# Kernel tuning notes

Hardware: AMD Instinct MI355X
Metric: run time of the kernel (lower is better)

## Reference

```python
import jax, jax.numpy as jnp
import numpy as np

N, E = 50000, 300000
IN_DIM, CODE_DIM = 1024, 768
HID, HEADS, DH = 256, 4, 64
NUM_REL = 5
CODE_WEIGHT = 1.0


def setup_inputs() -> dict:
    key = jax.random.key(0)
    ks = jax.random.split(key, 24)
    p = lambda k, shape: jax.random.normal(k, shape, dtype=jnp.float32) * 0.05
    return {
        "x": jax.random.normal(ks[0], (N, IN_DIM), dtype=jnp.float32),
        "edge_index": jax.random.randint(ks[1], (2, E), 0, N, dtype=jnp.int64),
        "edge_type": jax.random.randint(ks[2], (E,), 0, NUM_REL, dtype=jnp.int64),
        "edge_weight": jax.random.uniform(ks[3], (E,), dtype=jnp.float32),
        "rel_emb": p(ks[4], (NUM_REL, HID)),
        "W_in": p(ks[5], (HID, IN_DIM)),
        "b_in": jnp.zeros((HID,), jnp.float32),
        "W1": p(ks[6], (HEADS * DH, HID)),
        "a1_src": p(ks[7], (HEADS, DH)),
        "a1_dst": p(ks[8], (HEADS, DH)),
        "b1": jnp.zeros((HEADS * DH,), jnp.float32),
        "W2": p(ks[9], (HEADS * DH, HID)),
        "a2_src": p(ks[10], (HEADS, DH)),
        "a2_dst": p(ks[11], (HEADS, DH)),
        "b2": jnp.zeros((HEADS * DH,), jnp.float32),
        "ln1_g": jnp.ones((HID,), jnp.float32),
        "ln1_b": jnp.zeros((HID,), jnp.float32),
        "ln2_g": jnp.ones((HID,), jnp.float32),
        "ln2_b": jnp.zeros((HID,), jnp.float32),
        "W_out": p(ks[12], (1, HID)),
        "b_out": jnp.zeros((1,), jnp.float32),
    }


def _layer_norm(x, g, b, eps=1e-5):
    m = x.mean(-1, keepdims=True)
    v = ((x - m) ** 2).mean(-1, keepdims=True)
    return (x - m) * jax.lax.rsqrt(v + eps) * g + b


def _gat_conv(h, s_all, d_all, W, a_src, a_dst, bias):
    # PyG GATConv (concat=True, negative_slope=0.2), self-loops already in s_all/d_all
    xh = (h @ W.T).reshape(N, HEADS, DH)                      # [N,H,DH]
    al_s = (xh * a_src).sum(-1)                                # [N,H]
    al_d = (xh * a_dst).sum(-1)                                # [N,H]
    e = jax.nn.leaky_relu(al_s[s_all] + al_d[d_all], 0.2)      # [E+N,H]
    mx = jax.ops.segment_max(e, d_all, num_segments=N)         # segment softmax over dst
    ex = jnp.exp(e - mx[d_all])
    den = jax.ops.segment_sum(ex, d_all, num_segments=N)
    alpha = ex / (den[d_all] + 1e-16)
    out = jax.ops.segment_sum(xh[s_all] * alpha[:, :, None], d_all, num_segments=N)
    return out.reshape(N, HEADS * DH) + bias


def reference(x, edge_index, edge_type, edge_weight, rel_emb, W_in, b_in,
              W1, a1_src, a1_dst, b1, W2, a2_src, a2_dst, b2,
              ln1_g, ln1_b, ln2_g, ln2_b, W_out, b_out):
    # split (code_at_front=True), standardize numeric, l2-normalize code
    x_code = x[:, :CODE_DIM]
    x_num = x[:, CODE_DIM:]
    m = x_num.mean(0, keepdims=True)
    s = jnp.maximum(x_num.std(0, ddof=1, keepdims=True), 1e-6)
    x_num = (x_num - m) / s
    nrm = jnp.maximum(jnp.linalg.norm(x_code, axis=1, keepdims=True), 1e-12)
    x_code = x_code / nrm
    xin = jnp.concatenate([x_num, CODE_WEIGHT * x_code], axis=-1)

    h = jax.nn.relu(xin @ W_in.T + b_in)                       # [N,HID]

    src, dst = edge_index[0], edge_index[1]
    rel = rel_emb[edge_type] * edge_weight[:, None]            # [E,HID]
    msg = h[src] + rel
    h = h.at[dst].add(msg)                                     # index_add

    loop = jnp.arange(N, dtype=src.dtype)                      # GATConv add_self_loops
    s_all = jnp.concatenate([src, loop])
    d_all = jnp.concatenate([dst, loop])

    h1 = _gat_conv(h, s_all, d_all, W1, a1_src, a1_dst, b1)
    h = _layer_norm(h1 + h, ln1_g, ln1_b)
    h2 = _gat_conv(h, s_all, d_all, W2, a2_src, a2_dst, b2)
    h = _layer_norm(h2 + h, ln2_g, ln2_b)
    return (h @ W_out.T + b_out).squeeze(-1)                   # [N]
```

## Files before the change

kernel.cpp:

```cpp
#include <hip/hip_runtime.h>
#include <math.h>

constexpr int NN   = 50000;
constexpr int EE   = 300000;
constexpr int IND  = 1024;
constexpr int CODE = 768;
constexpr int HID  = 256;

typedef __bf16 bf16_t;
typedef bf16_t bf16x4 __attribute__((ext_vector_type(4)));
typedef bf16_t bf16x8 __attribute__((ext_vector_type(8)));
typedef float  f32x4  __attribute__((ext_vector_type(4)));

__device__ __forceinline__ f32x4 mfma16(bf16x8 a, bf16x8 b, f32x4 c) {
    return __builtin_amdgcn_mfma_f32_16x16x32_bf16(a, b, c, 0, 0, 0);
}

#define GLOAD_LDS16(gp, lp) __builtin_amdgcn_global_load_lds(                         \
    (__attribute__((address_space(1))) void*)(gp),                                    \
    (__attribute__((address_space(3))) void*)(lp), 16, 0, 0)

__device__ __forceinline__ void cvt_split(f32x4 u0, f32x4 u1, bf16x8& hi, bf16x8& lo) {
    #pragma unroll
    for (int i = 0; i < 4; i++) {
        bf16_t h0 = (bf16_t)u0[i];
        hi[i]     = h0;
        lo[i]     = (bf16_t)(u0[i] - (float)h0);
        bf16_t h1 = (bf16_t)u1[i];
        hi[4 + i] = h1;
        lo[4 + i] = (bf16_t)(u1[i] - (float)h1);
    }
}

__device__ __forceinline__ f32x4 ld_bf4(const bf16_t* p) {
    bf16x4 v = *(const bf16x4*)p;
    f32x4 r;
    r[0] = (float)v[0]; r[1] = (float)v[1]; r[2] = (float)v[2]; r[3] = (float)v[3];
    return r;
}

__global__ void colstats_kernel(const float* __restrict__ x, float* __restrict__ sums) {
    int col = threadIdx.x;
    float s = 0.f, s2 = 0.f;
    for (int row = blockIdx.x; row < NN; row += gridDim.x) {
        float v = x[(size_t)row * IND + CODE + col];
        s += v; s2 += v * v;
    }
    atomicAdd(&sums[col], s);
    atomicAdd(&sums[256 + col], s2);
}

__global__ void rownorm_kernel(const float* __restrict__ x, float* __restrict__ invnorm) {
    int lane = threadIdx.x & 63;
    int wid  = threadIdx.x >> 6;
    int row  = blockIdx.x * 4 + wid;
    if (row >= NN) return;
    const float4* x4 = (const float4*)(x + (size_t)row * IND);
    float s = 0.f;
    #pragma unroll
    for (int i = 0; i < 3; i++) {
        float4 v = x4[lane + i * 64];
        s += v.x * v.x + v.y * v.y + v.z * v.z + v.w * v.w;
    }
    #pragma unroll
    for (int off = 32; off; off >>= 1) s += __shfl_xor(s, off);
    if (lane == 0) invnorm[row] = 1.f / fmaxf(sqrtf(s), 1e-12f);
}

__global__ void prep_w_kernel(const float* __restrict__ W, const float* __restrict__ sums,
                              const float* __restrict__ b_in, bf16_t* __restrict__ Wh,
                              float* __restrict__ cb)
{
    int c = blockIdx.x, t = threadIdx.x;
    float mean = sums[t] / (float)NN;
    float var  = (sums[256 + t] - (float)NN * mean * mean) / (float)(NN - 1);
    float sd   = fmaxf(sqrtf(fmaxf(var, 0.f)), 1e-6f);
    float invstd = 1.f / sd;

    const float* wr = W + (size_t)c * IND;
    bf16_t* wh = Wh + (size_t)c * IND;
    for (int k = t; k < 768; k += 256) wh[k] = (bf16_t)wr[256 + k];
    wh[768 + t] = (bf16_t)(wr[t] * invstd);

    float p = wr[t] * invstd * mean;
    #pragma unroll
    for (int off = 32; off; off >>= 1) p += __shfl_xor(p, off);
    __shared__ float ps[4];
    if ((t & 63) == 0) ps[t >> 6] = p;
    __syncthreads();
    if (t == 0) cb[c] = b_in[c] - (ps[0] + ps[1] + ps[2] + ps[3]);
}

__global__ void prep_ws_kernel(const float* __restrict__ W1, const float* __restrict__ W2,
                               bf16_t* __restrict__ Wh1, bf16_t* __restrict__ Wh2)
{
    int c = blockIdx.x, t = threadIdx.x;
    if (c < 256) Wh1[(size_t)c * 256 + t] = (bf16_t)W1[(size_t)c * 256 + t];
    else {
        int cc = c - 256;
        Wh2[(size_t)cc * 256 + t] = (bf16_t)W2[(size_t)cc * 256 + t];
    }
}


__device__ __forceinline__ void stage_a(const float* __restrict__ src, int ldk,
                                        int rowbase, int maxrow, int k0,
                                        float* ldsbuf, int tid) {
    int w = tid >> 6, l = tid & 63;
    int lr = l >> 3, lc = l & 7;
    int g  = lc ^ lr;
    #pragma unroll
    for (int i = 0; i < 4; i++) {
        int rloc = i * 32 + w * 8;
        float* dst = ldsbuf + rloc * 32;
        int row = rowbase + rloc + lr;
        if (row > maxrow) row = maxrow;
        const float* gp = src + (size_t)row * ldk + k0 + g * 4;
        GLOAD_LDS16(gp, dst);
    }
}

__device__ __forceinline__ void stage_b(const bf16_t* __restrict__ src, int n0, int ldk,
                                        int maxrow, int k0, bf16_t* buf, int tid) {
    int w = tid >> 6, l = tid & 63;
    #pragma unroll
    for (int i = 0; i < 2; i++) {
        int gbase = w * 128 + i * 64;
        bf16_t* dst = buf + gbase * 8;
        int g = gbase + l;
        int col = g >> 2, p = g & 3;
        int gs = p ^ ((col >> 1) & 3);
        int row = n0 + col;
        if (row > maxrow) row = maxrow;
        const bf16_t* gp = src + (size_t)row * ldk + k0 + gs * 8;
        GLOAD_LDS16(gp, dst);
    }
}

template<int MODE, int K, int FATTN>
__global__ __launch_bounds__(256) void gemm_mfma_kernel(
    const float* __restrict__ A, const bf16_t* __restrict__ A16,
    const bf16_t* __restrict__ Bh, const float* __restrict__ cb,
    const float* __restrict__ invnorm, const float* __restrict__ a_src,
    const float* __restrict__ a_dst, float* __restrict__ out,
    bf16_t* __restrict__ xhb, float* __restrict__ al_s, float* __restrict__ al_d)
{
    constexpr int ASZF = (MODE == 1) ? 2 * 128 * 32 : 8;
    constexpr int ASZB = (MODE == 0) ? 2 * 128 * 32 : 8;
    __shared__ float  Asf[ASZF];
    __shared__ bf16_t Asb[ASZB];
    __shared__ bf16_t Bhs[2][128 * 32];
    __shared__ float inv_s[128];
    constexpr int NT = K / 32;

    int tid  = threadIdx.x;
    int lane = tid & 63;
    int w    = tid >> 6;
    int wr   = w >> 1, wc = w & 1;
    int r0   = blockIdx.x * 128, n0 = blockIdx.y * 128;

    if (MODE == 1 && tid < 128) {
        int r = r0 + tid;
        inv_s[tid] = (r < NN) ? invnorm[r] : 1.f;
    }

    f32x4 acc[4][4];
    #pragma unroll
    for (int i = 0; i < 4; i++)
        #pragma unroll
        for (int j = 0; j < 4; j++) acc[i][j] = (f32x4)0.f;

    int kc = lane >> 4, fr = lane & 15;

    if (MODE == 1) stage_a(A, K, r0, NN - 1, 0, Asf, tid);
    else           stage_b(A16, r0, K, NN - 1, 0, Asb, tid);
    stage_b(Bh, n0, K, 255, 0, Bhs[0], tid);
    __syncthreads();

    for (int t = 0; t < NT; ++t) {
        int buf = t & 1;
        if (t + 1 < NT) {
            if (MODE == 1) stage_a(A, K, r0, NN - 1, (t + 1) * 32, Asf + (buf ^ 1) * (128 * 32), tid);
            else           stage_b(A16, r0, K, NN - 1, (t + 1) * 32, Asb + (buf ^ 1) * (128 * 32), tid);
            stage_b(Bh, n0, K, 255, (t + 1) * 32, Bhs[buf ^ 1], tid);
        }
        if (MODE == 1 && t == 24) {
            #pragma unroll
            for (int mf = 0; mf < 4; mf++) {
                f32x4 iv = *(const f32x4*)&inv_s[wr * 64 + mf * 16 + kc * 4];
                #pragma unroll
                for (int nf = 0; nf < 4; nf++)
                    #pragma unroll
                    for (int j = 0; j < 4; j++) acc[mf][nf][j] *= iv[j];
            }
        }
        const bf16_t* Hb = Bhs[buf];
        bf16x8 ahi[4], alo[4];
        #pragma unroll
        for (int mf = 0; mf < 4; mf++) {
            int r = wr * 64 + mf * 16 + fr;
            if (MODE == 1) {
                const float* Ab = Asf + buf * (128 * 32);
                int rb = r * 32, r7 = r & 7;
                f32x4 u0 = *(const f32x4*)&Ab[rb + (((2 * kc + 0) ^ r7) << 2)];
                f32x4 u1 = *(const f32x4*)&Ab[rb + (((2 * kc + 1) ^ r7) << 2)];
                cvt_split(u0, u1, ahi[mf], alo[mf]);
            } else {
                const bf16_t* Ab = Asb + buf * (128 * 32);
                int pr = kc ^ ((r >> 1) & 3);
                ahi[mf] = *(const bf16x8*)&Ab[r * 32 + pr * 8];
            }
        }
        #pragma unroll
        for (int nf = 0; nf < 4; nf++) {
            int c  = wc * 64 + nf * 16 + fr;
            int pr = kc ^ ((c >> 1) & 3);
            bf16x8 bhi = *(const bf16x8*)&Hb[c * 32 + pr * 8];
            #pragma unroll
            for (int mf = 0; mf < 4; mf++) {
                acc[mf][nf] = mfma16(ahi[mf], bhi, acc[mf][nf]);
                if (MODE == 1) acc[mf][nf] = mfma16(alo[mf], bhi, acc[mf][nf]);
            }
        }
        __syncthreads();
    }

    int head = blockIdx.y * 2 + wc;
    float asv[4], adv[4];
    if (FATTN) {
        #pragma unroll
        for (int nf = 0; nf < 4; nf++) {
            asv[nf] = a_src[head * 64 + nf * 16 + fr];
            adv[nf] = a_dst[head * 64 + nf * 16 + fr];
        }
    }
    #pragma unroll
    for (int mf = 0; mf < 4; mf++) {
        #pragma unroll
        for (int j = 0; j < 4; j++) {
            int row = r0 + wr * 64 + mf * 16 + kc * 4 + j;
            bool ok = row < NN;
            float s = 0.f, d = 0.f;
            #pragma unroll
            for (int nf = 0; nf < 4; nf++) {
                int col = n0 + wc * 64 + nf * 16 + fr;
                float v = acc[mf][nf][j];
                if (MODE == 1) {
                    v = fmaxf(v + cb[col], 0.f);
                    if (ok) out[(size_t)row * HID + col] = v;
                }
                if (FATTN) {
                    s += v * asv[nf]; d += v * adv[nf];
                    if (ok) xhb[(size_t)row * HID + col] = (bf16_t)v;
                }
            }
            if (FATTN) {
                #pragma unroll
                for (int off = 1; off < 16; off <<= 1) {
                    s += __shfl_xor(s, off);
                    d += __shfl_xor(d, off);
                }
                if (ok && fr == 0) {
                    al_s[row * 4 + head] = s;
                    al_d[row * 4 + head] = d;
                }
            }
        }
    }
}

__global__ void deg_kernel(const int* __restrict__ ei, int* __restrict__ deg) {
    int e = blockIdx.x * 256 + threadIdx.x;
    if (e < EE) atomicAdd(&deg[ei[EE + e]], 1);
}

constexpr int SCB = 1024;
constexpr int SCN = (NN + SCB - 1) / SCB;

__global__ void scan_pass1(const int* __restrict__ deg, int* __restrict__ bsum) {
    int b = blockIdx.x, t = threadIdx.x;
    int base = b * SCB + t * 4;
    int s = 0;
    #pragma unroll
    for (int i = 0; i < 4; i++) { int idx = base + i; if (idx < NN) s += deg[idx]; }
    #pragma unroll
    for (int off = 32; off; off >>= 1) s += __shfl_xor(s, off);
    __shared__ int ps[4];
    if ((t & 63) == 0) ps[t >> 6] = s;
    __syncthreads();
    if (t == 0) bsum[b] = ps[0] + ps[1] + ps[2] + ps[3];
}

__global__ void scan_pass2(int* __restrict__ bsum) {
    int t = threadIdx.x;
    int orig = (t < SCN) ? bsum[t] : 0;
    int v = orig;
    for (int off = 1; off < 64; off <<= 1) {
        int u = __shfl_up(v, off);
        if (t >= off) v += u;
    }
    if (t < SCN) bsum[t] = v - orig;
}

__global__ void scan_pass3(const int* __restrict__ deg, const int* __restrict__ boffs,
                           int* __restrict__ row_ptr, int* __restrict__ cursor) {
    int b = blockIdx.x, t = threadIdx.x;
    int base = b * SCB + t * 4;
    int d[4]; int tot = 0;
    #pragma unroll
    for (int i = 0; i < 4; i++) { int idx = base + i; d[i] = (idx < NN) ? deg[idx] : 0; tot += d[i]; }
    int v = tot;
    for (int off = 1; off < 64; off <<= 1) {
        int u = __shfl_up(v, off);
        if ((t & 63) >= off) v += u;
    }
    __shared__ int wsum[4];
    if ((t & 63) == 63) wsum[t >> 6] = v;
    __syncthreads();
    int woff = 0;
    for (int j = 0; j < (t >> 6); j++) woff += wsum[j];
    int run = boffs[b] + woff + v - tot;
    #pragma unroll
    for (int i = 0; i < 4; i++) {
        int idx = base + i;
        if (idx < NN) {
            cursor[idx] = run;
            run += d[i];
            row_ptr[idx + 1] = run;
        }
    }
    if (b == 0 && t == 0) row_ptr[0] = 0;
}

__global__ void fill_kernel(const int* __restrict__ ei, const int* __restrict__ etype,
                            const float* __restrict__ ew, int* __restrict__ cursor,
                            int* __restrict__ csr_src, int* __restrict__ csr_t,
                            float* __restrict__ csr_w) {
    int e = blockIdx.x * 256 + threadIdx.x;
    if (e >= EE) return;
    int dst = ei[EE + e];
    int pos = atomicAdd(&cursor[dst], 1);
    csr_src[pos] = ei[e];
    csr_t[pos]   = etype[e];
    csr_w[pos]   = ew[e];
}

__global__ void relagg_kernel(const float* __restrict__ h, const int* __restrict__ row_ptr,
                              const int* __restrict__ csr_src, const int* __restrict__ csr_t,
                              const float* __restrict__ csr_w,
                              const float* __restrict__ rel_emb, float* __restrict__ out,
                              bf16_t* __restrict__ out16)
{
    int lane = threadIdx.x & 63, wid = threadIdx.x >> 6;
    int node = blockIdx.x * 4 + wid;
    if (node >= NN) return;
    int c0 = lane * 4;
    f32x4 acc = *(const f32x4*)(h + (size_t)node * HID + c0);
    float wsum[5] = {0.f, 0.f, 0.f, 0.f, 0.f};
    int beg = row_ptr[node], end = row_ptr[node + 1];
    for (int k = beg; k < end; k += 8) {
        int s[8], tt[8]; float ww[8], vm[8];
        #pragma unroll
        for (int j = 0; j < 8; j++) {
            int kk = k + j;
            bool valid = kk < end;
            kk = valid ? kk : (end - 1);
            s[j]  = csr_src[kk];
            tt[j] = csr_t[kk];
            ww[j] = valid ? csr_w[kk] : 0.f;
            vm[j] = valid ? 1.f : 0.f;
        }
        f32x4 xv[8];
        #pragma unroll
        for (int j = 0; j < 8; j++) xv[j] = *(const f32x4*)(h + (size_t)s[j] * HID + c0);
        #pragma unroll
        for (int j = 0; j < 8; j++) {
            acc += vm[j] * xv[j];
            #pragma unroll
            for (int r = 0; r < 5; r++) wsum[r] += (tt[j] == r) ? ww[j] : 0.f;
        }
    }
    #pragma unroll
    for (int r = 0; r < 5; r++)
        acc += wsum[r] * *(const f32x4*)(rel_emb + r * HID + c0);
    *(f32x4*)(out + (size_t)node * HID + c0) = acc;
    bf16x4 a16;
    #pragma unroll
    for (int i = 0; i < 4; i++) a16[i] = (bf16_t)acc[i];
    *(bf16x4*)(out16 + (size_t)node * HID + c0) = a16;
}

template<int FINAL>
__global__ void gat_kernel(const bf16_t* __restrict__ xhb, const float* __restrict__ al_s,
                           const float* __restrict__ al_d, const int* __restrict__ row_ptr,
                           const int* __restrict__ csr_src, const float* __restrict__ h_res,
                           const float* __restrict__ bias, const float* __restrict__ ln_g,
                           const float* __restrict__ ln_b, float* __restrict__ out,
                           bf16_t* __restrict__ out16,
                           const float* __restrict__ W_out, const float* __restrict__ b_out,
                           float* __restrict__ final_out)
{
    int lane = threadIdx.x & 63, wid = threadIdx.x >> 6;
    int node = blockIdx.x * 4 + wid;
    if (node >= NN) return;
    int hh = lane >> 4;
    int c0 = lane * 4;

    float ald = al_d[node * 4 + hh];
    float m, den;
    f32x4 acc;

    {
        float als = al_s[node * 4 + hh];
        float e = als + ald;
        e = (e >= 0.f) ? e : 0.2f * e;
        m = e; den = 1.f;
        acc = ld_bf4(xhb + (size_t)node * HID + c0);
    }

    int beg = row_ptr[node], end = row_ptr[node + 1];
    for (int k = beg; k < end; k += 8) {
        int s[8]; float als[8];
        #pragma unroll
        for (int j = 0; j < 8; j++) {
            int kk = k + j;
            bool valid = kk < end;
            s[j] = csr_src[valid ? kk : (end - 1)];
            als[j] = valid ? 0.f : -INFINITY;
        }
        #pragma unroll
        for (int j = 0; j < 8; j++)
            if (als[j] == 0.f) als[j] = al_s[s[j] * 4 + hh];
        f32x4 xv[8];
        #pragma unroll
        for (int j = 0; j < 8; j++) xv[j] = ld_bf4(xhb + (size_t)s[j] * HID + c0);
        #pragma unroll
        for (int j = 0; j < 8; j++) {
            float e = als[j] + ald;
            e = (e >= 0.f) ? e : 0.2f * e;
            float mn  = fmaxf(m, e);
            float f   = __expf(m - mn);
            float wgt = __expf(e - mn);
            m   = mn;
            den = den * f + wgt;
            acc = acc * f + wgt * xv[j];
        }
    }

    f32x4 bia = *(const f32x4*)(bias + c0);
    f32x4 res = *(const f32x4*)(h_res + (size_t)node * HID + c0);
    f32x4 z;
    float rd = 1.f / (den + 1e-16f);
    #pragma unroll
    for (int i = 0; i < 4; i++) z[i] = acc[i] * rd + bia[i] + res[i];

    float s = z[0] + z[1] + z[2] + z[3];
    #pragma unroll
    for (int off = 32; off; off >>= 1) s += __shfl_xor(s, off);
    float mean = s * (1.f / 256.f);
    float vp = 0.f;
    #pragma unroll
    for (int i = 0; i < 4; i++) { float d2 = z[i] - mean; vp += d2 * d2; }
    #pragma unroll
    for (int off = 32; off; off >>= 1) vp += __shfl_xor(vp, off);
    float rstd = rsqrtf(vp * (1.f / 256.f) + 1e-5f);

    f32x4 g = *(const f32x4*)(ln_g + c0);
    f32x4 bb = *(const f32x4*)(ln_b + c0);
    if (FINAL) {
        f32x4 wo = *(const f32x4*)(W_out + c0);
        float dot = 0.f;
        #pragma unroll
        for (int i = 0; i < 4; i++)
            dot += ((z[i] - mean) * rstd * g[i] + bb[i]) * wo[i];
        #pragma unroll
        for (int off = 32; off; off >>= 1) dot += __shfl_xor(dot, off);
        if (lane == 0) final_out[node] = dot + b_out[0];
    } else {
        f32x4 o;
        bf16x4 o16;
        #pragma unroll
        for (int i = 0; i < 4; i++) {
            o[i] = (z[i] - mean) * rstd * g[i] + bb[i];
            o16[i] = (bf16_t)o[i];
        }
        *(f32x4*)(out + (size_t)node * HID + c0) = o;
        *(bf16x4*)(out16 + (size_t)node * HID + c0) = o16;
    }
}

extern "C" void kernel_launch(void* const* d_in, const int* in_sizes, int n_in,
                              void* d_out, int out_size, void* d_ws, size_t ws_size,
                              hipStream_t stream) {
    const float* x       = (const float*)d_in[0];
    const int*   ei      = (const int*)d_in[1];
    const int*   etype   = (const int*)d_in[2];
    const float* ew      = (const float*)d_in[3];
    const float* rel_emb = (const float*)d_in[4];
    const float* W_in    = (const float*)d_in[5];
    const float* b_in    = (const float*)d_in[6];
    const float* W1      = (const float*)d_in[7];
    const float* a1s     = (const float*)d_in[8];
    const float* a1d     = (const float*)d_in[9];
    const float* b1      = (const float*)d_in[10];
    const float* W2      = (const float*)d_in[11];
    const float* a2s     = (const float*)d_in[12];
    const float* a2d     = (const float*)d_in[13];
    const float* b2      = (const float*)d_in[14];
    const float* ln1g    = (const float*)d_in[15];
    const float* ln1b    = (const float*)d_in[16];
    const float* ln2g    = (const float*)d_in[17];
    const float* ln2b    = (const float*)d_in[18];
    const float* W_out   = (const float*)d_in[19];
    const float* b_out   = (const float*)d_in[20];
    float* out = (float*)d_out;

    char* ws = (char*)d_ws;
    auto alloc = [&](size_t bytes) {
        void* p = (void*)ws;
        ws += (bytes + 255) & ~(size_t)255;
        return p;
    };
    float*  bufA     = (float*)alloc((size_t)NN * HID * 4);
    float*  bufB     = (float*)alloc((size_t)NN * HID * 4);
    bf16_t* xhb      = (bf16_t*)alloc((size_t)NN * HID * 2);
    bf16_t* gin16    = (bf16_t*)alloc((size_t)NN * HID * 2);
    bf16_t* wmh      = (bf16_t*)alloc((size_t)HID * IND * 2);
    bf16_t* w1h      = (bf16_t*)alloc((size_t)HID * HID * 2);
    bf16_t* w2h      = (bf16_t*)alloc((size_t)HID * HID * 2);
    float*  cbv      = (float*)alloc(256 * 4);
    float*  stats_s  = (float*)alloc(512 * 4);
    float*  invnorm  = (float*)alloc((size_t)NN * 4);
    float*  al_s     = (float*)alloc((size_t)NN * 4 * 4);
    float*  al_d     = (float*)alloc((size_t)NN * 4 * 4);
    int*    deg      = (int*)alloc((size_t)NN * 4);
    int*    row_ptr  = (int*)alloc((size_t)(NN + 1) * 4);
    int*    cursor   = (int*)alloc((size_t)NN * 4);
    int*    csr_src  = (int*)alloc((size_t)EE * 4);
    int*    csr_t    = (int*)alloc((size_t)EE * 4);
    float*  csr_w    = (float*)alloc((size_t)EE * 4);
    int*    bsum     = (int*)alloc(64 * 4);

    hipMemsetAsync(stats_s, 0, 512 * 4, stream);
    hipMemsetAsync(deg, 0, (size_t)NN * 4, stream);

    colstats_kernel<<<1024, 256, 0, stream>>>(x, stats_s);
    rownorm_kernel<<<(NN + 3) / 4, 256, 0, stream>>>(x, invnorm);
    prep_w_kernel<<<256, 256, 0, stream>>>(W_in, stats_s, b_in, wmh, cbv);
    prep_ws_kernel<<<512, 256, 0, stream>>>(W1, W2, w1h, w2h);

    deg_kernel<<<(EE + 255) / 256, 256, 0, stream>>>(ei, deg);
    scan_pass1<<<SCN, 256, 0, stream>>>(deg, bsum);
    scan_pass2<<<1, 64, 0, stream>>>(bsum);
    scan_pass3<<<SCN, 256, 0, stream>>>(deg, bsum, row_ptr, cursor);
    fill_kernel<<<(EE + 255) / 256, 256, 0, stream>>>(ei, etype, ew, cursor,
                                                      csr_src, csr_t, csr_w);

    dim3 g1((NN + 127) / 128, 2);

    gemm_mfma_kernel<1, 1024, 0><<<g1, 256, 0, stream>>>(
        x, nullptr, wmh, cbv, invnorm, nullptr, nullptr, bufA, nullptr, nullptr, nullptr);

    int nodeBlocks = (NN + 3) / 4;

    relagg_kernel<<<nodeBlocks, 256, 0, stream>>>(bufA, row_ptr, csr_src, csr_t, csr_w,
                                                  rel_emb, bufB, gin16);

    gemm_mfma_kernel<0, 256, 1><<<g1, 256, 0, stream>>>(
        nullptr, gin16, w1h, nullptr, nullptr, a1s, a1d, nullptr, xhb, al_s, al_d);
    gat_kernel<0><<<nodeBlocks, 256, 0, stream>>>(xhb, al_s, al_d, row_ptr, csr_src,
                                                  bufB, b1, ln1g, ln1b, bufA, gin16,
                                                  nullptr, nullptr, nullptr);

    gemm_mfma_kernel<0, 256, 1><<<g1, 256, 0, stream>>>(
        nullptr, gin16, w2h, nullptr, nullptr, a2s, a2d, nullptr, xhb, al_s, al_d);
    gat_kernel<1><<<nodeBlocks, 256, 0, stream>>>(xhb, al_s, al_d, row_ptr, csr_src,
                                                  bufA, b2, ln2g, ln2b, nullptr, nullptr,
                                                  W_out, b_out, out);
}
```

Before: 427.7 us.

## Pre-normalize input to bf16 and drop split-precision MFMA in input GEMM

A new xin_kernel applies the row L2 norm to the code columns and column standardization to the numeric columns, writing a bf16 copy of the input with the numeric block placed first. The input projection GEMM then streams bf16 A tiles with single MFMAs, where it previously loaded fp32 tiles and did hi/lo split conversion with two MFMAs per fragment. Folding the stats into the weights and bias is dropped, and the weight conversions are merged into one kernel. This trades an extra read of x plus a bf16 write and re-read of about 100 MB against halving MFMA work and fp32 A traffic, and it lowers input precision to plain bf16.

```diff
diff --git a/kernel.cpp b/kernel.cpp
--- a/kernel.cpp
+++ b/kernel.cpp
@@ -19,18 +19,6 @@
 #define GLOAD_LDS16(gp, lp) __builtin_amdgcn_global_load_lds(                         \
     (__attribute__((address_space(1))) void*)(gp),                                    \
     (__attribute__((address_space(3))) void*)(lp), 16, 0, 0)
-
-__device__ __forceinline__ void cvt_split(f32x4 u0, f32x4 u1, bf16x8& hi, bf16x8& lo) {
-    #pragma unroll
-    for (int i = 0; i < 4; i++) {
-        bf16_t h0 = (bf16_t)u0[i];
-        hi[i]     = h0;
-        lo[i]     = (bf16_t)(u0[i] - (float)h0);
-        bf16_t h1 = (bf16_t)u1[i];
-        hi[4 + i] = h1;
-        lo[4 + i] = (bf16_t)(u1[i] - (float)h1);
-    }
-}
 
 __device__ __forceinline__ f32x4 ld_bf4(const bf16_t* p) {
     bf16x4 v = *(const bf16x4*)p;
@@ -50,75 +38,63 @@
     atomicAdd(&sums[256 + col], s2);
 }
 
-__global__ void rownorm_kernel(const float* __restrict__ x, float* __restrict__ invnorm) {
-    int lane = threadIdx.x & 63;
-    int wid  = threadIdx.x >> 6;
+__global__ void xin_kernel(const float* __restrict__ x, const float* __restrict__ sums,
+                           bf16_t* __restrict__ xin)
+{
+    int lane = threadIdx.x & 63, wid = threadIdx.x >> 6;
     int row  = blockIdx.x * 4 + wid;
     if (row >= NN) return;
-    const float4* x4 = (const float4*)(x + (size_t)row * IND);
+    const f32x4* x4 = (const f32x4*)(x + (size_t)row * IND);
+    f32x4 v[4];
+    #pragma unroll
+    for (int i = 0; i < 4; i++) v[i] = x4[lane + 64 * i];
     float s = 0.f;
     #pragma unroll
+    for (int i = 0; i < 3; i++)
+        s += v[i][0] * v[i][0] + v[i][1] * v[i][1] + v[i][2] * v[i][2] + v[i][3] * v[i][3];
+    #pragma unroll
+    for (int off = 32; off; off >>= 1) s += __shfl_xor(s, off);
+    float inr = 1.f / fmaxf(sqrtf(s), 1e-12f);
+
+    bf16_t* xr = xin + (size_t)row * IND;
+    #pragma unroll
     for (int i = 0; i < 3; i++) {
-        float4 v = x4[lane + i * 64];
-        s += v.x * v.x + v.y * v.y + v.z * v.z + v.w * v.w;
-    }
-    #pragma unroll
-    for (int off = 32; off; off >>= 1) s += __shfl_xor(s, off);
-    if (lane == 0) invnorm[row] = 1.f / fmaxf(sqrtf(s), 1e-12f);
-}
-
-__global__ void prep_w_kernel(const float* __restrict__ W, const float* __restrict__ sums,
-                              const float* __restrict__ b_in, bf16_t* __restrict__ Wh,
-                              float* __restrict__ cb)
+        bf16x4 o;
+        #pragma unroll
+        for (int q = 0; q < 4; q++) o[q] = (bf16_t)(v[i][q] * inr);
+        *(bf16x4*)(xr + 256 + 4 * (lane + 64 * i)) = o;
+    }
+    {
+        bf16x4 o;
+        #pragma unroll
+        for (int q = 0; q < 4; q++) {
+            int j = 4 * lane + q;
+            float mean = sums[j] / (float)NN;
+            float var  = (sums[256 + j] - (float)NN * mean * mean) / (float)(NN - 1);
+            float invstd = 1.f / fmaxf(sqrtf(fmaxf(var, 0.f)), 1e-6f);
+            o[q] = (bf16_t)((v[3][q] - mean) * invstd);
+        }
+        *(bf16x4*)(xr + 4 * lane) = o;
+    }
+}
+
+__global__ void prep_all_kernel(const float* __restrict__ W_in, const float* __restrict__ W1,
+                                const float* __restrict__ W2, bf16_t* __restrict__ Wmh,
+                                bf16_t* __restrict__ Wh1, bf16_t* __restrict__ Wh2)
 {
-    int c = blockIdx.x, t = threadIdx.x;
-    float mean = sums[t] / (float)NN;
-    float var  = (sums[256 + t] - (float)NN * mean * mean) / (float)(NN - 1);
-    float sd   = fmaxf(sqrtf(fmaxf(var, 0.f)), 1e-6f);
-    float invstd = 1.f / sd;
-
-    const float* wr = W + (size_t)c * IND;
-    bf16_t* wh = Wh + (size_t)c * IND;
-    for (int k = t; k < 768; k += 256) wh[k] = (bf16_t)wr[256 + k];
-    wh[768 + t] = (bf16_t)(wr[t] * invstd);
-
-    float p = wr[t] * invstd * mean;
-    #pragma unroll
-    for (int off = 32; off; off >>= 1) p += __shfl_xor(p, off);
-    __shared__ float ps[4];
-    if ((t & 63) == 0) ps[t >> 6] = p;
-    __syncthreads();
-    if (t == 0) cb[c] = b_in[c] - (ps[0] + ps[1] + ps[2] + ps[3]);
-}
-
-__global__ void prep_ws_kernel(const float* __restrict__ W1, const float* __restrict__ W2,
-                               bf16_t* __restrict__ Wh1, bf16_t* __restrict__ Wh2)
-{
-    int c = blockIdx.x, t = threadIdx.x;
-    if (c < 256) Wh1[(size_t)c * 256 + t] = (bf16_t)W1[(size_t)c * 256 + t];
-    else {
-        int cc = c - 256;
-        Wh2[(size_t)cc * 256 + t] = (bf16_t)W2[(size_t)cc * 256 + t];
-    }
-}
-
-
-__device__ __forceinline__ void stage_a(const float* __restrict__ src, int ldk,
-                                        int rowbase, int maxrow, int k0,
-                                        float* ldsbuf, int tid) {
-    int w = tid >> 6, l = tid & 63;
-    int lr = l >> 3, lc = l & 7;
-    int g  = lc ^ lr;
-    #pragma unroll
-    for (int i = 0; i < 4; i++) {
-        int rloc = i * 32 + w * 8;
-        float* dst = ldsbuf + rloc * 32;
-        int row = rowbase + rloc + lr;
-        if (row > maxrow) row = maxrow;
-        const float* gp = src + (size_t)row * ldk + k0 + g * 4;
-        GLOAD_LDS16(gp, dst);
-    }
-}
+    int b = blockIdx.x, t = threadIdx.x;
+    if (b < 1024) {
+        size_t i = (size_t)b * 256 + t;
+        Wmh[i] = (bf16_t)W_in[i];
+    } else if (b < 1280) {
+        size_t i = (size_t)(b - 1024) * 256 + t;
+        Wh1[i] = (bf16_t)W1[i];
+    } else {
+        size_t i = (size_t)(b - 1280) * 256 + t;
+        Wh2[i] = (bf16_t)W2[i];
+    }
+}
+
 
 __device__ __forceinline__ void stage_b(const bf16_t* __restrict__ src, int n0, int ldk,
                                         int maxrow, int k0, bf16_t* buf, int tid) {
@@ -139,18 +115,13 @@
 
 template<int MODE, int K, int FATTN>
 __global__ __launch_bounds__(256) void gemm_mfma_kernel(
-    const float* __restrict__ A, const bf16_t* __restrict__ A16,
-    const bf16_t* __restrict__ Bh, const float* __restrict__ cb,
-    const float* __restrict__ invnorm, const float* __restrict__ a_src,
+    const bf16_t* __restrict__ A16, const bf16_t* __restrict__ Bh,
+    const float* __restrict__ bin, const float* __restrict__ a_src,
     const float* __restrict__ a_dst, float* __restrict__ out,
     bf16_t* __restrict__ xhb, float* __restrict__ al_s, float* __restrict__ al_d)
 {
-    constexpr int ASZF = (MODE == 1) ? 2 * 128 * 32 : 8;
-    constexpr int ASZB = (MODE == 0) ? 2 * 128 * 32 : 8;
-    __shared__ float  Asf[ASZF];
-    __shared__ bf16_t Asb[ASZB];
+    __shared__ bf16_t Asb[2][128 * 32];
     __shared__ bf16_t Bhs[2][128 * 32];
-    __shared__ float inv_s[128];
     constexpr int NT = K / 32;
 
     int tid  = threadIdx.x;
@@ -159,11 +130,6 @@
     int wr   = w >> 1, wc = w & 1;
     int r0   = blockIdx.x * 128, n0 = blockIdx.y * 128;
 
-    if (MODE == 1 && tid < 128) {
-        int r = r0 + tid;
-        inv_s[tid] = (r < NN) ? invnorm[r] : 1.f;
-    }
-
     f32x4 acc[4][4];
     #pragma unroll
     for (int i = 0; i < 4; i++)
@@ -172,44 +138,24 @@
 
     int kc = lane >> 4, fr = lane & 15;
 
-    if (MODE == 1) stage_a(A, K, r0, NN - 1, 0, Asf, tid);
-    else           stage_b(A16, r0, K, NN - 1, 0, Asb, tid);
+    stage_b(A16, r0, K, NN - 1, 0, Asb[0], tid);
     stage_b(Bh, n0, K, 255, 0, Bhs[0], tid);
     __syncthreads();
 
     for (int t = 0; t < NT; ++t) {
         int buf = t & 1;
         if (t + 1 < NT) {
-            if (MODE == 1) stage_a(A, K, r0, NN - 1, (t + 1) * 32, Asf + (buf ^ 1) * (128 * 32), tid);
-            else           stage_b(A16, r0, K, NN - 1, (t + 1) * 32, Asb + (buf ^ 1) * (128 * 32), tid);
+            stage_b(A16, r0, K, NN - 1, (t + 1) * 32, Asb[buf ^ 1], tid);
             stage_b(Bh, n0, K, 255, (t + 1) * 32, Bhs[buf ^ 1], tid);
         }
-        if (MODE == 1 && t == 24) {
-            #pragma unroll
-            for (int mf = 0; mf < 4; mf++) {
-                f32x4 iv = *(const f32x4*)&inv_s[wr * 64 + mf * 16 + kc * 4];
-                #pragma unroll
-                for (int nf = 0; nf < 4; nf++)
-                    #pragma unroll
-                    for (int j = 0; j < 4; j++) acc[mf][nf][j] *= iv[j];
-            }
-        }
+        const bf16_t* Ab = Asb[buf];
         const bf16_t* Hb = Bhs[buf];
-        bf16x8 ahi[4], alo[4];
+        bf16x8 ahi[4];
         #pragma unroll
         for (int mf = 0; mf < 4; mf++) {
-            int r = wr * 64 + mf * 16 + fr;
-            if (MODE == 1) {
-                const float* Ab = Asf + buf * (128 * 32);
-                int rb = r * 32, r7 = r & 7;
-                f32x4 u0 = *(const f32x4*)&Ab[rb + (((2 * kc + 0) ^ r7) << 2)];
-                f32x4 u1 = *(const f32x4*)&Ab[rb + (((2 * kc + 1) ^ r7) << 2)];
-                cvt_split(u0, u1, ahi[mf], alo[mf]);
-            } else {
-                const bf16_t* Ab = Asb + buf * (128 * 32);
-                int pr = kc ^ ((r >> 1) & 3);
-                ahi[mf] = *(const bf16x8*)&Ab[r * 32 + pr * 8];
-            }
+            int r  = wr * 64 + mf * 16 + fr;
+            int pr = kc ^ ((r >> 1) & 3);
+            ahi[mf] = *(const bf16x8*)&Ab[r * 32 + pr * 8];
         }
         #pragma unroll
         for (int nf = 0; nf < 4; nf++) {
@@ -217,10 +163,8 @@
             int pr = kc ^ ((c >> 1) & 3);
             bf16x8 bhi = *(const bf16x8*)&Hb[c * 32 + pr * 8];
             #pragma unroll
-            for (int mf = 0; mf < 4; mf++) {
+            for (int mf = 0; mf < 4; mf++)
                 acc[mf][nf] = mfma16(ahi[mf], bhi, acc[mf][nf]);
-                if (MODE == 1) acc[mf][nf] = mfma16(alo[mf], bhi, acc[mf][nf]);
-            }
         }
         __syncthreads();
     }
@@ -246,7 +190,7 @@
                 int col = n0 + wc * 64 + nf * 16 + fr;
                 float v = acc[mf][nf][j];
                 if (MODE == 1) {
-                    v = fmaxf(v + cb[col], 0.f);
+                    v = fmaxf(v + bin[col], 0.f);
                     if (ok) out[(size_t)row * HID + col] = v;
                 }
                 if (FATTN) {
@@ -523,14 +467,13 @@
     };
     float*  bufA     = (float*)alloc((size_t)NN * HID * 4);
     float*  bufB     = (float*)alloc((size_t)NN * HID * 4);
+    bf16_t* xin16    = (bf16_t*)alloc((size_t)NN * IND * 2);
     bf16_t* xhb      = (bf16_t*)alloc((size_t)NN * HID * 2);
     bf16_t* gin16    = (bf16_t*)alloc((size_t)NN * HID * 2);
     bf16_t* wmh      = (bf16_t*)alloc((size_t)HID * IND * 2);
     bf16_t* w1h      = (bf16_t*)alloc((size_t)HID * HID * 2);
     bf16_t* w2h      = (bf16_t*)alloc((size_t)HID * HID * 2);
-    float*  cbv      = (float*)alloc(256 * 4);
     float*  stats_s  = (float*)alloc(512 * 4);
-    float*  invnorm  = (float*)alloc((size_t)NN * 4);
     float*  al_s     = (float*)alloc((size_t)NN * 4 * 4);
     float*  al_d     = (float*)alloc((size_t)NN * 4 * 4);
     int*    deg      = (int*)alloc((size_t)NN * 4);
@@ -545,9 +488,8 @@
     hipMemsetAsync(deg, 0, (size_t)NN * 4, stream);
 
     colstats_kernel<<<1024, 256, 0, stream>>>(x, stats_s);
-    rownorm_kernel<<<(NN + 3) / 4, 256, 0, stream>>>(x, invnorm);
-    prep_w_kernel<<<256, 256, 0, stream>>>(W_in, stats_s, b_in, wmh, cbv);
-    prep_ws_kernel<<<512, 256, 0, stream>>>(W1, W2, w1h, w2h);
+    xin_kernel<<<(NN + 3) / 4, 256, 0, stream>>>(x, stats_s, xin16);
+    prep_all_kernel<<<1536, 256, 0, stream>>>(W_in, W1, W2, wmh, w1h, w2h);
 
     deg_kernel<<<(EE + 255) / 256, 256, 0, stream>>>(ei, deg);
     scan_pass1<<<SCN, 256, 0, stream>>>(deg, bsum);
@@ -559,7 +501,7 @@
     dim3 g1((NN + 127) / 128, 2);
 
     gemm_mfma_kernel<1, 1024, 0><<<g1, 256, 0, stream>>>(
-        x, nullptr, wmh, cbv, invnorm, nullptr, nullptr, bufA, nullptr, nullptr, nullptr);
+        xin16, wmh, b_in, nullptr, nullptr, bufA, nullptr, nullptr, nullptr);
 
     int nodeBlocks = (NN + 3) / 4;
 
@@ -567,13 +509,13 @@
                                                   rel_emb, bufB, gin16);
 
     gemm_mfma_kernel<0, 256, 1><<<g1, 256, 0, stream>>>(
-        nullptr, gin16, w1h, nullptr, nullptr, a1s, a1d, nullptr, xhb, al_s, al_d);
+        gin16, w1h, nullptr, a1s, a1d, nullptr, xhb, al_s, al_d);
     gat_kernel<0><<<nodeBlocks, 256, 0, stream>>>(xhb, al_s, al_d, row_ptr, csr_src,
                                                   bufB, b1, ln1g, ln1b, bufA, gin16,
                                                   nullptr, nullptr, nullptr);
 
     gemm_mfma_kernel<0, 256, 1><<<g1, 256, 0, stream>>>(
-        nullptr, gin16, w2h, nullptr, nullptr, a2s, a2d, nullptr, xhb, al_s, al_d);
+        gin16, w2h, nullptr, a2s, a2d, nullptr, xhb, al_s, al_d);
     gat_kernel<1><<<nodeBlocks, 256, 0, stream>>>(xhb, al_s, al_d, row_ptr, csr_src,
                                                   bufA, b2, ln2g, ln2b, nullptr, nullptr,
                                                   W_out, b_out, out);
```

Result: faster. 417.1 us (-2.5%).
